# Kernel optimization log

Measured on AMD Instinct MI355X. Metric: run time of the kernel, lower is better.

Reference implementation:

```python
import jax, jax.numpy as jnp
import numpy as np

P = 1024
D_FF = 4096
TGT = 4096
SRC = 4096


def _ln(x, g, b, eps=1e-5):
    mu = jnp.mean(x, axis=-1, keepdims=True)
    var = jnp.mean((x - mu) ** 2, axis=-1, keepdims=True)
    return (x - mu) / jnp.sqrt(var + eps) * g + b


def setup_inputs() -> dict:
    key = jax.random.key(0)
    ks = jax.random.split(key, 32)
    s = 1.0 / np.sqrt(P)
    sf = 1.0 / np.sqrt(D_FF)
    d = {
        "Y": jax.random.normal(ks[0], (TGT, P), jnp.float32),
        "Xp": jax.random.normal(ks[1], (SRC, P), jnp.float32),
        # self-attn projections (Linear: y = x @ W + b, W stored [in, out])
        "wq1": jax.random.uniform(ks[2], (P, P), jnp.float32, -s, s),
        "bq1": jnp.zeros((P,), jnp.float32),
        "wk1": jax.random.uniform(ks[3], (P, P), jnp.float32, -s, s),
        "bk1": jnp.zeros((P,), jnp.float32),
        "wv1": jax.random.uniform(ks[4], (P, P), jnp.float32, -s, s),
        "bv1": jnp.zeros((P,), jnp.float32),
        "w0": jax.random.uniform(ks[5], (P, P), jnp.float32, -s, s),
        "b0": jnp.zeros((P,), jnp.float32),
        "g1": jnp.ones((P,), jnp.float32),
        "be1": jnp.zeros((P,), jnp.float32),
        # cross-attn projections
        "wq2": jax.random.uniform(ks[6], (P, P), jnp.float32, -s, s),
        "bq2": jnp.zeros((P,), jnp.float32),
        "wk2": jax.random.uniform(ks[7], (P, P), jnp.float32, -s, s),
        "bk2": jnp.zeros((P,), jnp.float32),
        "wv2": jax.random.uniform(ks[8], (P, P), jnp.float32, -s, s),
        "bv2": jnp.zeros((P,), jnp.float32),
        "w1": jax.random.uniform(ks[9], (P, P), jnp.float32, -s, s),
        "b1": jnp.zeros((P,), jnp.float32),
        "g2": jnp.ones((P,), jnp.float32),
        "be2": jnp.zeros((P,), jnp.float32),
        # FFN
        "w2": jax.random.uniform(ks[10], (P, D_FF), jnp.float32, -s, s),
        "b2": jnp.zeros((D_FF,), jnp.float32),
        "w3": jax.random.uniform(ks[11], (D_FF, P), jnp.float32, -sf, sf),
        "b3": jnp.zeros((P,), jnp.float32),
        "g3": jnp.ones((P,), jnp.float32),
        "be3": jnp.zeros((P,), jnp.float32),
    }
    return d


def reference(Y, Xp, wq1, bq1, wk1, bk1, wv1, bv1, w0, b0, g1, be1,
              wq2, bq2, wk2, bk2, wv2, bv2, w1, b1, g2, be2,
              w2, b2, w3, b3, g3, be3):
    m = Y.shape[0]
    scale = 1.0 / jnp.sqrt(jnp.asarray(P, Y.dtype))
    # --- masked self-attention on Y ---
    Q = Y @ wq1 + bq1            # [m, p]
    K = Y @ wk1 + bk1
    V = Y @ wv1 + bv1
    S = (Q @ K.T) * scale        # [m, m]
    causal = jnp.tril(jnp.ones((m, m), bool))
    S = jnp.where(causal, S, jnp.asarray(-1e9, S.dtype))
    A = jax.nn.softmax(S, axis=-1)
    T1 = (A @ V) @ w0 + b0
    U1 = _ln(Y + T1, g1, be1)
    # --- cross-attention with encoder output Xp ---
    Q = U1 @ wq2 + bq2           # [m, p]
    K = Xp @ wk2 + bk2           # [n, p]
    V = Xp @ wv2 + bv2
    S = (Q @ K.T) * scale        # [m, n]
    A = jax.nn.softmax(S, axis=-1)
    T2 = (A @ V) @ w1 + b1
    U2 = _ln(U1 + T2, g2, be2)
    # --- position-wise FFN ---
    Z = jax.nn.relu(U2 @ w2 + b2) @ w3 + b3
    U3 = _ln(U2 + Z, g3, be3)
    return U3
```

## Files before the change

kernel.cpp:

```cpp
#include <hip/hip_runtime.h>
#include <hip/hip_bf16.h>

typedef __bf16 bf16x8 __attribute__((ext_vector_type(8)));
typedef __bf16 bf16x4 __attribute__((ext_vector_type(4)));
typedef float f32x4 __attribute__((ext_vector_type(4)));

#define AS1P(p) ((__attribute__((address_space(1))) void*)(void*)(p))
#define AS3P(p) ((__attribute__((address_space(3))) void*)(p))

__global__ __launch_bounds__(256, 3) void gemm_bt(
    const __hip_bfloat16* __restrict__ A, int lda,
    const __hip_bfloat16* __restrict__ Bt, int ldb,
    int M, int N, int K, int ldc,
    const float* __restrict__ bias, int bias_mode,
    float scale,
    const float* __restrict__ residual,
    int relu, int causal_skip, int trapezoid, int ksplit,
    float* __restrict__ Cf, __hip_bfloat16* __restrict__ Cb,
    int nsplit1, const __hip_bfloat16* __restrict__ A2,
    const __hip_bfloat16* __restrict__ Bt2, int ldb2, int ldc2,
    const float* __restrict__ bias2, __hip_bfloat16* __restrict__ Cb2)
{
    int nb = blockIdx.x;
    int mb = blockIdx.y;
    {
        const int gx = gridDim.x, gy = gridDim.y;
        if ((gx & 3) == 0 && (gy & 1) == 0) {
            const int id = mb * gx + nb;
            const int X  = id & 7;
            const int L  = id >> 3;
            const int rn = gx >> 2, rm = gy >> 1;
            const int nb_l = L / rm, mb_l = L - nb_l * rm;
            nb = (X & 3) * rn + nb_l;
            mb = (X >> 2) * rm + mb_l;
        }
    }
    if (nsplit1 && nb >= nsplit1) {
        A = A2; Bt = Bt2; ldb = ldb2; ldc = ldc2; bias = bias2;
        Cb = Cb2; Cf = nullptr; residual = nullptr;
        nb -= nsplit1;
    }
    const int m_base = mb * 128;
    const int n_base = nb * 128;
    if (causal_skip && (n_base > m_base + 127)) return;
    int Kend = K;
    if (trapezoid) { int kl = m_base + 128; Kend = kl < K ? kl : K; }
    int kb = 0, ke = Kend;
    if (ksplit) {
        kb = blockIdx.z * ksplit;
        int k2 = kb + ksplit; ke = k2 < Kend ? k2 : Kend;
        if (kb >= ke) return;
        Cb += (size_t)blockIdx.z * M * ldc;
        Cf = nullptr;
    }
    const int nt = (ke - kb) >> 5;

    __shared__ __align__(16) __hip_bfloat16 Lds[3][8192];

    const int tid  = threadIdx.x;
    const int lane = tid & 63;
    const int wave = tid >> 6;
    const int wm = (wave >> 1) * 64;
    const int wn = (wave & 1) * 64;

    f32x4 acc[4][4];
#pragma unroll
    for (int i = 0; i < 4; ++i)
#pragma unroll
        for (int j = 0; j < 4; ++j) acc[i][j] = f32x4{0.f, 0.f, 0.f, 0.f};

    const bool isA = wave < 2;
    const __hip_bfloat16* G = isA ? (A + (size_t)m_base * lda) : (Bt + (size_t)n_base * ldb);
    const int ldg = isA ? lda : ldb;
    const int q0 = (wave & 1) * 4;
    const int rsub = lane >> 2;
    const int cx   = (lane & 3) ^ ((lane >> 3) & 3);
    const size_t grow = (size_t)(q0 * 16 + rsub) * ldg + (size_t)cx * 8 + kb;
    const int ldsoff = (isA ? 0 : 4096) + q0 * 512;

    const int lrow = lane & 15;
    const int cph  = ((lane >> 4) ^ ((lrow >> 1) & 3)) * 8;

#define ISSUE_TILE(KT, STG)                                                      \
    {                                                                            \
        const __hip_bfloat16* g = G + grow + (size_t)(KT) * 32;                  \
        __hip_bfloat16* dst = &Lds[STG][ldsoff];                                 \
        _Pragma("unroll")                                                        \
        for (int q = 0; q < 4; ++q) {                                            \
            __builtin_amdgcn_global_load_lds(AS1P(g), AS3P(dst), 16, 0, 0);      \
            g += (size_t)16 * ldg; dst += 512;                                   \
        }                                                                        \
    }

    ISSUE_TILE(0, 0)
    if (nt > 1) ISSUE_TILE(1, 1)

    int cur = 0;
    for (int kt = 0; kt < nt; ++kt) {
        __builtin_amdgcn_sched_barrier(0);
        if (kt + 1 < nt) __builtin_amdgcn_s_waitcnt(0x0F74);
        else             __builtin_amdgcn_s_waitcnt(0x0F70);
        __builtin_amdgcn_sched_barrier(0);
        __builtin_amdgcn_s_barrier();
        __builtin_amdgcn_sched_barrier(0);
        if (kt + 2 < nt) {
            int s2 = cur + 2; if (s2 >= 3) s2 -= 3;
            ISSUE_TILE(kt + 2, s2)
        }

        bf16x8 af[4], bfv[4];
#pragma unroll
        for (int i = 0; i < 4; ++i)
            af[i] = *(const bf16x8*)&Lds[cur][(wm + i * 16 + lrow) * 32 + cph];
#pragma unroll
        for (int j = 0; j < 4; ++j)
            bfv[j] = *(const bf16x8*)&Lds[cur][4096 + (wn + j * 16 + lrow) * 32 + cph];
#pragma unroll
        for (int i = 0; i < 4; ++i)
#pragma unroll
            for (int j = 0; j < 4; ++j)
                acc[i][j] = __builtin_amdgcn_mfma_f32_16x16x32_bf16(af[i], bfv[j], acc[i][j], 0, 0, 0);

        cur = (cur + 1 == 3) ? 0 : cur + 1;
    }
#undef ISSUE_TILE

    const int r0 = (lane >> 4) * 4;
    const int c0 = lane & 15;
#pragma unroll
    for (int i = 0; i < 4; ++i) {
#pragma unroll
        for (int j = 0; j < 4; ++j) {
            const int col = n_base + wn + j * 16 + c0;
#pragma unroll
            for (int r = 0; r < 4; ++r) {
                const int row = m_base + wm + i * 16 + r0 + r;
                float v = acc[i][j][r] * scale;
                if (bias_mode == 1) v += bias[col];
                else if (bias_mode == 2) v += bias[row];
                if (relu) v = fmaxf(v, 0.f);
                const size_t idx = (size_t)row * ldc + col;
                if (residual) v += residual[idx];
                if (Cf) Cf[idx] = v;
                else    Cb[idx] = __float2bfloat16(v);
            }
        }
    }
}

__global__ __launch_bounds__(256) void reduce_k_kernel(
    const __hip_bfloat16* __restrict__ Pb, int M, int N, int nsplit, int KC, int trapK,
    const float* __restrict__ bias, const float* __restrict__ residual,
    float* __restrict__ Cf, __hip_bfloat16* __restrict__ Cb)
{
    const int idx = blockIdx.x * 256 + threadIdx.x;
    const int nv = N >> 2;
    const int row = idx / nv;
    if (row >= M) return;
    const int c4 = (idx - row * nv) * 4;
    int nc = nsplit;
    if (trapK) {
        int kend = (row & ~127) + 128; if (kend > trapK) kend = trapK;
        nc = (kend + KC - 1) / KC;
    }
    float s0 = 0.f, s1 = 0.f, s2 = 0.f, s3 = 0.f;
    for (int c = 0; c < nc; ++c) {
        const bf16x4 p = *(const bf16x4*)(Pb + ((size_t)c * M + row) * N + c4);
        s0 += (float)p[0]; s1 += (float)p[1]; s2 += (float)p[2]; s3 += (float)p[3];
    }
    if (bias) {
        const f32x4 b = *(const f32x4*)(bias + c4);
        s0 += b[0]; s1 += b[1]; s2 += b[2]; s3 += b[3];
    }
    if (residual) {
        const f32x4 rv = *(const f32x4*)(residual + (size_t)row * N + c4);
        s0 += rv[0]; s1 += rv[1]; s2 += rv[2]; s3 += rv[3];
    }
    if (Cf) { f32x4 o = {s0, s1, s2, s3}; *(f32x4*)(Cf + (size_t)row * N + c4) = o; }
    else {
        bf16x4 o = { (__bf16)s0, (__bf16)s1, (__bf16)s2, (__bf16)s3 };
        *(bf16x4*)(Cb + (size_t)row * N + c4) = o;
    }
}

__global__ __launch_bounds__(256) void convert_bf16_kernel(
    const float* __restrict__ x, __hip_bfloat16* __restrict__ y, int n4)
{
    const int i = blockIdx.x * 256 + threadIdx.x;
    if (i >= n4) return;
    const float4 v = ((const float4*)x)[i];
    bf16x4 o = { (__bf16)v.x, (__bf16)v.y, (__bf16)v.z, (__bf16)v.w };
    *(bf16x4*)(y + (size_t)i * 4) = o;
}

__global__ __launch_bounds__(256) void transpose_convert_kernel(
    const float* __restrict__ W, __hip_bfloat16* __restrict__ Wt, int K, int N)
{
    __shared__ float t[32][33];
    const int k0 = blockIdx.y * 32;
    const int n0 = blockIdx.x * 32;
    const int tx = threadIdx.x;
    for (int i = threadIdx.y; i < 32; i += 8)
        t[i][tx] = W[(size_t)(k0 + i) * N + n0 + tx];
    __syncthreads();
    for (int i = threadIdx.y; i < 32; i += 8)
        Wt[(size_t)(n0 + i) * K + k0 + tx] = __float2bfloat16(t[tx][i]);
}

__global__ __launch_bounds__(256) void transpose_bf16_kernel(
    const __hip_bfloat16* __restrict__ src, int ls,
    __hip_bfloat16* __restrict__ dst, int ld)
{
    __shared__ __hip_bfloat16 t[32][33];
    const int r0 = blockIdx.y * 32;
    const int c0 = blockIdx.x * 32;
    const int tx = threadIdx.x;
    for (int i = threadIdx.y; i < 32; i += 8)
        t[i][tx] = src[(size_t)(r0 + i) * ls + c0 + tx];
    __syncthreads();
    for (int i = threadIdx.y; i < 32; i += 8)
        dst[(size_t)(c0 + i) * ld + r0 + tx] = t[tx][i];
}

__global__ __launch_bounds__(256) void softmax_kernel(
    const __hip_bfloat16* __restrict__ S, __hip_bfloat16* __restrict__ A, int N, int causal)
{
    __shared__ float sm[4];
    const int row = blockIdx.x;
    const int tid = threadIdx.x;
    const int limit = causal ? (row + 1) : N;
    const int zlimit = causal ? (((row & ~127) + 128) < N ? ((row & ~127) + 128) : N) : N;
    const __hip_bfloat16* Srow = S + (size_t)row * N;
    __hip_bfloat16* Arow = A + (size_t)row * N;
    const int nv = limit >> 2;

    float m = -3.0e38f;
    for (int v = tid; v < nv; v += 256) {
        const bf16x4 x = *(const bf16x4*)(Srow + (size_t)v * 4);
        m = fmaxf(m, fmaxf(fmaxf((float)x[0], (float)x[1]), fmaxf((float)x[2], (float)x[3])));
    }
    for (int j = (nv << 2) + tid; j < limit; j += 256) m = fmaxf(m, (float)Srow[j]);
#pragma unroll
    for (int o = 32; o; o >>= 1) m = fmaxf(m, __shfl_down(m, o));
    if ((tid & 63) == 0) sm[tid >> 6] = m;
    __syncthreads();
    m = fmaxf(fmaxf(sm[0], sm[1]), fmaxf(sm[2], sm[3]));
    __syncthreads();

    float s = 0.f;
    for (int v = tid; v < nv; v += 256) {
        const bf16x4 x = *(const bf16x4*)(Srow + (size_t)v * 4);
        s += __expf((float)x[0] - m) + __expf((float)x[1] - m)
           + __expf((float)x[2] - m) + __expf((float)x[3] - m);
    }
    for (int j = (nv << 2) + tid; j < limit; j += 256) s += __expf((float)Srow[j] - m);
#pragma unroll
    for (int o = 32; o; o >>= 1) s += __shfl_down(s, o);
    if ((tid & 63) == 0) sm[tid >> 6] = s;
    __syncthreads();
    s = sm[0] + sm[1] + sm[2] + sm[3];
    const float inv = 1.f / s;

    for (int v = tid; v < nv; v += 256) {
        const bf16x4 x = *(const bf16x4*)(Srow + (size_t)v * 4);
        bf16x4 o = { (__bf16)(__expf((float)x[0] - m) * inv), (__bf16)(__expf((float)x[1] - m) * inv),
                     (__bf16)(__expf((float)x[2] - m) * inv), (__bf16)(__expf((float)x[3] - m) * inv) };
        *(bf16x4*)(Arow + (size_t)v * 4) = o;
    }
    for (int j = (nv << 2) + tid; j < limit; j += 256)
        Arow[j] = __float2bfloat16(__expf((float)Srow[j] - m) * inv);
    const __hip_bfloat16 z = __float2bfloat16(0.f);
    for (int j = limit + tid; j < zlimit; j += 256) Arow[j] = z;
}

__global__ __launch_bounds__(256) void layernorm_kernel(
    const float* __restrict__ X, const float* __restrict__ g, const float* __restrict__ b,
    float* __restrict__ outF, __hip_bfloat16* __restrict__ outB)
{
    __shared__ float sm[8];
    const int row = blockIdx.x;
    const int tid = threadIdx.x;
    const float4 v = ((const float4*)(X + (size_t)row * 1024))[tid];
    float s  = v.x + v.y + v.z + v.w;
    float ss = v.x * v.x + v.y * v.y + v.z * v.z + v.w * v.w;
#pragma unroll
    for (int o = 32; o; o >>= 1) { s += __shfl_down(s, o); ss += __shfl_down(ss, o); }
    if ((tid & 63) == 0) { sm[tid >> 6] = s; sm[4 + (tid >> 6)] = ss; }
    __syncthreads();
    s  = sm[0] + sm[1] + sm[2] + sm[3];
    ss = sm[4] + sm[5] + sm[6] + sm[7];
    const float mu   = s * (1.f / 1024.f);
    const float var  = ss * (1.f / 1024.f) - mu * mu;
    const float rstd = rsqrtf(var + 1e-5f);
    const float4 gv = ((const float4*)g)[tid];
    const float4 bv = ((const float4*)b)[tid];
    float4 o;
    o.x = (v.x - mu) * rstd * gv.x + bv.x;
    o.y = (v.y - mu) * rstd * gv.y + bv.y;
    o.z = (v.z - mu) * rstd * gv.z + bv.z;
    o.w = (v.w - mu) * rstd * gv.w + bv.w;
    ((float4*)(outF + (size_t)row * 1024))[tid] = o;
    if (outB) {
        bf16x4 ob = { (__bf16)o.x, (__bf16)o.y, (__bf16)o.z, (__bf16)o.w };
        *(bf16x4*)(outB + (size_t)row * 1024 + (size_t)tid * 4) = ob;
    }
}

extern "C" void kernel_launch(void* const* d_in, const int* in_sizes, int n_in,
                              void* d_out, int out_size, void* d_ws, size_t ws_size,
                              hipStream_t stream)
{
    const int M = 4096, Pd = 1024, DFF = 4096, NS = 4096;
    const size_t MB = 1024 * 1024;

    const float* Y   = (const float*)d_in[0];
    const float* Xp  = (const float*)d_in[1];
    const float* wq1 = (const float*)d_in[2];  const float* bq1 = (const float*)d_in[3];
    const float* wk1 = (const float*)d_in[4];  const float* bk1 = (const float*)d_in[5];
    const float* wv1 = (const float*)d_in[6];  const float* bv1 = (const float*)d_in[7];
    const float* w0  = (const float*)d_in[8];  const float* b0  = (const float*)d_in[9];
    const float* g1  = (const float*)d_in[10]; const float* be1 = (const float*)d_in[11];
    const float* wq2 = (const float*)d_in[12]; const float* bq2 = (const float*)d_in[13];
    const float* wk2 = (const float*)d_in[14]; const float* bk2 = (const float*)d_in[15];
    const float* wv2 = (const float*)d_in[16]; const float* bv2 = (const float*)d_in[17];
    const float* w1  = (const float*)d_in[18]; const float* b1  = (const float*)d_in[19];
    const float* g2  = (const float*)d_in[20]; const float* be2 = (const float*)d_in[21];
    const float* w2  = (const float*)d_in[22]; const float* b2  = (const float*)d_in[23];
    const float* w3  = (const float*)d_in[24]; const float* b3  = (const float*)d_in[25];
    const float* g3  = (const float*)d_in[26]; const float* be3 = (const float*)d_in[27];

    char* ws = (char*)d_ws;
    __hip_bfloat16* Ybf   = (__hip_bfloat16*)(ws + 0 * MB);
    __hip_bfloat16* Ubf   = (__hip_bfloat16*)(ws + 0 * MB);
    __hip_bfloat16* Xpbf  = (__hip_bfloat16*)(ws + 8 * MB);
    __hip_bfloat16* AVbf  = (__hip_bfloat16*)(ws + 8 * MB);
    __hip_bfloat16* Qbf   = (__hip_bfloat16*)(ws + 8 * MB);
    __hip_bfloat16* wqkv1t= (__hip_bfloat16*)(ws + 16 * MB);
    __hip_bfloat16* w0t   = (__hip_bfloat16*)(ws + 22 * MB);
    __hip_bfloat16* wq2t  = (__hip_bfloat16*)(ws + 24 * MB);
    __hip_bfloat16* wkv2t = (__hip_bfloat16*)(ws + 26 * MB);
    __hip_bfloat16* w1t   = (__hip_bfloat16*)(ws + 30 * MB);
    __hip_bfloat16* w2t   = (__hip_bfloat16*)(ws + 32 * MB);
    __hip_bfloat16* w3t   = (__hip_bfloat16*)(ws + 40 * MB);
    float*          bqkv1 = (float*)(ws + 48 * MB);
    float*          bkv2  = (float*)(ws + 48 * MB + 512 * 1024);
    __hip_bfloat16* QKV1  = (__hip_bfloat16*)(ws + 49 * MB);
    __hip_bfloat16* KV2   = (__hip_bfloat16*)(ws + 73 * MB);
    __hip_bfloat16* Vt    = (__hip_bfloat16*)(ws + 89 * MB);
    __hip_bfloat16* Sb    = (__hip_bfloat16*)(ws + 97 * MB);
    __hip_bfloat16* Pb    = (__hip_bfloat16*)(ws + 97 * MB);
    __hip_bfloat16* Abf   = (__hip_bfloat16*)(ws + 161 * MB);
    float*          Xres  = (float*)(ws + 193 * MB);
    float*          Uf    = (float*)(ws + 209 * MB);
    float*          Out   = (float*)d_out;
    if (ws_size < 225 * MB) return;

    auto cvt = [&](const float* src, __hip_bfloat16* dst, int n) {
        convert_bf16_kernel<<<dim3(n / 1024), dim3(256), 0, stream>>>(src, dst, n / 4);
    };
    auto tconv = [&](const float* W, __hip_bfloat16* Wt, int K, int N) {
        transpose_convert_kernel<<<dim3(N / 32, K / 32), dim3(32, 8), 0, stream>>>(W, Wt, K, N);
    };
    auto tbf = [&](const __hip_bfloat16* src, int ls, __hip_bfloat16* dst, int ld, int R, int C) {
        transpose_bf16_kernel<<<dim3(C / 32, R / 32), dim3(32, 8), 0, stream>>>(src, ls, dst, ld);
    };
    auto gemm = [&](const __hip_bfloat16* A, int lda, const __hip_bfloat16* Bt, int ldb,
                    int Mm, int Nn, int Kk, int ldc,
                    const float* bias, int bmode, float scale, const float* res,
                    int relu, int causal, int trap, int ksplit,
                    float* Cf, __hip_bfloat16* Cb) {
        const int nz = ksplit ? (Kk + ksplit - 1) / ksplit : 1;
        gemm_bt<<<dim3(Nn / 128, Mm / 128, nz), dim3(256), 0, stream>>>(
            A, lda, Bt, ldb, Mm, Nn, Kk, ldc, bias, bmode, scale, res, relu, causal, trap, ksplit,
            Cf, Cb, 0, nullptr, nullptr, 0, 0, nullptr, nullptr);
    };
    auto reduce = [&](const __hip_bfloat16* P, int Mm, int Nn, int nsplit, int KC, int trapK,
                      const float* bias, const float* res, float* Cf, __hip_bfloat16* Cb) {
        reduce_k_kernel<<<dim3(Mm * Nn / 1024), dim3(256), 0, stream>>>(
            P, Mm, Nn, nsplit, KC, trapK, bias, res, Cf, Cb);
    };

    const float scl = 0.03125f;

    cvt(Y,  Ybf,  M * Pd);
    cvt(Xp, Xpbf, NS * Pd);
    tconv(wq1, wqkv1t,            Pd, Pd);
    tconv(wk1, wqkv1t + Pd * Pd,  Pd, Pd);
    tconv(wv1, wqkv1t + 2*Pd*Pd,  Pd, Pd);
    tconv(w0,  w0t,  Pd, Pd);
    tconv(wq2, wq2t, Pd, Pd);
    tconv(wk2, wkv2t,           Pd, Pd);
    tconv(wv2, wkv2t + Pd * Pd, Pd, Pd);
    tconv(w1,  w1t,  Pd, Pd);
    tconv(w2, w2t, Pd, DFF);
    tconv(w3, w3t, DFF, Pd);
    hipMemcpyAsync(bqkv1,            bq1, Pd * 4, hipMemcpyDeviceToDevice, stream);
    hipMemcpyAsync(bqkv1 + Pd,       bk1, Pd * 4, hipMemcpyDeviceToDevice, stream);
    hipMemcpyAsync(bqkv1 + 2 * Pd,   bv1, Pd * 4, hipMemcpyDeviceToDevice, stream);
    hipMemcpyAsync(bkv2,             bk2, Pd * 4, hipMemcpyDeviceToDevice, stream);
    hipMemcpyAsync(bkv2 + Pd,        bv2, Pd * 4, hipMemcpyDeviceToDevice, stream);

    gemm_bt<<<dim3(40, 32, 1), dim3(256), 0, stream>>>(
        Ybf, Pd, wqkv1t, Pd, M, 3072, Pd, 3072, bqkv1, 1, 1.f, nullptr, 0, 0, 0, 0,
        nullptr, QKV1,
        24, Xpbf, wkv2t, Pd, 2048, bkv2, KV2);

    tbf(QKV1 + 2048, 3072, Vt, M, M, Pd);
    gemm(QKV1, 3072, QKV1 + 1024, 3072, M, M, Pd, M,
         nullptr, 0, scl, nullptr, 0, 1, 0, 0, nullptr, Sb);
    softmax_kernel<<<dim3(M), dim3(256), 0, stream>>>(Sb, Abf, M, 1);
    gemm(Abf, M, Vt, M, M, Pd, M, Pd,
         nullptr, 0, 1.f, nullptr, 0, 0, 1, 1024, nullptr, Pb);
    reduce(Pb, M, Pd, 4, 1024, M, nullptr, nullptr, nullptr, AVbf);
    gemm(AVbf, Pd, w0t, Pd, M, Pd, Pd, Pd,
         nullptr, 0, 1.f, nullptr, 0, 0, 0, 512, nullptr, Pb);
    reduce(Pb, M, Pd, 2, 512, 0, b0, Y, Xres, nullptr);
    layernorm_kernel<<<dim3(M), dim3(256), 0, stream>>>(Xres, g1, be1, Uf, Ubf);

    gemm(Ubf, Pd, wq2t, Pd, M, Pd, Pd, Pd,
         nullptr, 0, 1.f, nullptr, 0, 0, 0, 512, nullptr, Pb);
    reduce(Pb, M, Pd, 2, 512, 0, bq2, nullptr, nullptr, Qbf);
    tbf(KV2 + 1024, 2048, Vt, NS, NS, Pd);
    gemm(Qbf, Pd, KV2, 2048, M, NS, Pd, NS,
         nullptr, 0, scl, nullptr, 0, 0, 0, 0, nullptr, Sb);
    softmax_kernel<<<dim3(M), dim3(256), 0, stream>>>(Sb, Abf, NS, 0);
    gemm(Abf, NS, Vt, NS, M, Pd, NS, Pd,
         nullptr, 0, 1.f, nullptr, 0, 0, 0, 1024, nullptr, Pb);
    reduce(Pb, M, Pd, 4, 1024, 0, nullptr, nullptr, nullptr, AVbf);
    gemm(AVbf, Pd, w1t, Pd, M, Pd, Pd, Pd,
         nullptr, 0, 1.f, nullptr, 0, 0, 0, 512, nullptr, Pb);
    reduce(Pb, M, Pd, 2, 512, 0, b1, Uf, Xres, nullptr);
    layernorm_kernel<<<dim3(M), dim3(256), 0, stream>>>(Xres, g2, be2, Uf, Ubf);

    gemm(Ubf, Pd, w2t, Pd, M, DFF, Pd, DFF, b2, 1, 1.f, nullptr, 1, 0, 0, 0, nullptr, Abf);
    gemm(Abf, DFF, w3t, DFF, M, Pd, DFF, Pd,
         nullptr, 0, 1.f, nullptr, 0, 0, 0, 1024, nullptr, Pb);
    reduce(Pb, M, Pd, 4, 1024, 0, b3, Uf, Xres, nullptr);
    layernorm_kernel<<<dim3(M), dim3(256), 0, stream>>>(Xres, g3, be3, Out, nullptr);
}
```

Measured before the change: 778.0 us.

## Add 256x128-tile GEMM kernel with grouped block swizzle for large GEMMs

```diff
diff --git a/kernel.cpp b/kernel.cpp
--- a/kernel.cpp
+++ b/kernel.cpp
@@ -148,6 +148,140 @@
     }
 }
 
+__global__ __launch_bounds__(256, 2) void gemm_bt2(
+    const __hip_bfloat16* __restrict__ A, int lda,
+    const __hip_bfloat16* __restrict__ Bt, int ldb,
+    int M, int N, int K, int ldc,
+    const float* __restrict__ bias, int bias_mode,
+    float scale,
+    int relu, int causal_skip, int trapezoid, int ksplit,
+    __hip_bfloat16* __restrict__ Cb)
+{
+    int nb = blockIdx.x;
+    int mb = blockIdx.y;
+    {
+        const int gx = gridDim.x, gy = gridDim.y;
+        if ((gx & 3) == 0 && (gy & 1) == 0) {
+            const int id = mb * gx + nb;
+            const int X  = id & 7;
+            const int L  = id >> 3;
+            const int rn = gx >> 2, rm = gy >> 1;
+            const int nb_l = L / rm, mb_l = L - nb_l * rm;
+            nb = (X & 3) * rn + nb_l;
+            mb = (X >> 2) * rm + mb_l;
+        }
+    }
+    const int m_base = mb * 256;
+    const int n_base = nb * 128;
+    if (causal_skip && (n_base > m_base + 255)) return;
+    int Kend = K;
+    if (trapezoid) { int kl = m_base + 256; Kend = kl < K ? kl : K; }
+    int kb = 0, ke = Kend;
+    if (ksplit) {
+        kb = blockIdx.z * ksplit;
+        int k2 = kb + ksplit; ke = k2 < Kend ? k2 : Kend;
+        if (kb >= ke) return;
+        Cb += (size_t)blockIdx.z * M * ldc;
+    }
+    const int nt = (ke - kb) >> 5;
+
+    __shared__ __align__(16) __hip_bfloat16 Lds[3][12288];
+
+    const int tid  = threadIdx.x;
+    const int lane = tid & 63;
+    const int wave = tid >> 6;
+    const int wm = wave * 64;
+    const int wtm = (wave >> 1) * 128;
+    const int wtn = (wave & 1) * 64;
+
+    f32x4 acc[8][4];
+#pragma unroll
+    for (int i = 0; i < 8; ++i)
+#pragma unroll
+        for (int j = 0; j < 4; ++j) acc[i][j] = f32x4{0.f, 0.f, 0.f, 0.f};
+
+    const int rsub = lane >> 2;
+    const int cx   = (lane & 3) ^ ((lane >> 3) & 3);
+    const __hip_bfloat16* GA = A  + (size_t)(m_base + wave * 64) * lda + (size_t)rsub * lda + (size_t)cx * 8 + kb;
+    const __hip_bfloat16* GB = Bt + (size_t)(n_base + wave * 32) * ldb + (size_t)rsub * ldb + (size_t)cx * 8 + kb;
+    const int ldsA = wave * 2048;
+    const int ldsB = 8192 + wave * 1024;
+
+    const int lrow = lane & 15;
+    const int cph  = ((lane >> 4) ^ ((lrow >> 1) & 3)) * 8;
+
+#define ISSUE_TILE2(KT, STG)                                                     \
+    {                                                                            \
+        const size_t ko = (size_t)(KT) * 32;                                     \
+        const __hip_bfloat16* ga = GA + ko;                                      \
+        __hip_bfloat16* da = &Lds[STG][ldsA];                                    \
+        _Pragma("unroll")                                                        \
+        for (int q = 0; q < 4; ++q) {                                            \
+            __builtin_amdgcn_global_load_lds(AS1P(ga), AS3P(da), 16, 0, 0);      \
+            ga += (size_t)16 * lda; da += 512;                                   \
+        }                                                                        \
+        const __hip_bfloat16* gb = GB + ko;                                      \
+        __hip_bfloat16* db = &Lds[STG][ldsB];                                    \
+        _Pragma("unroll")                                                        \
+        for (int q = 0; q < 2; ++q) {                                            \
+            __builtin_amdgcn_global_load_lds(AS1P(gb), AS3P(db), 16, 0, 0);      \
+            gb += (size_t)16 * ldb; db += 512;                                   \
+        }                                                                        \
+    }
+
+    ISSUE_TILE2(0, 0)
+    if (nt > 1) ISSUE_TILE2(1, 1)
+
+    int cur = 0;
+    for (int kt = 0; kt < nt; ++kt) {
+        __builtin_amdgcn_sched_barrier(0);
+        if (kt + 1 < nt) __builtin_amdgcn_s_waitcnt(0x0F76);
+        else             __builtin_amdgcn_s_waitcnt(0x0F70);
+        __builtin_amdgcn_sched_barrier(0);
+        __builtin_amdgcn_s_barrier();
+        __builtin_amdgcn_sched_barrier(0);
+        if (kt + 2 < nt) {
+            int s2 = cur + 2; if (s2 >= 3) s2 -= 3;
+            ISSUE_TILE2(kt + 2, s2)
+        }
+
+        bf16x8 af[8], bfv[4];
+#pragma unroll
+        for (int i = 0; i < 8; ++i)
+            af[i] = *(const bf16x8*)&Lds[cur][(wtm + i * 16 + lrow) * 32 + cph];
+#pragma unroll
+        for (int j = 0; j < 4; ++j)
+            bfv[j] = *(const bf16x8*)&Lds[cur][8192 + (wtn + j * 16 + lrow) * 32 + cph];
+#pragma unroll
+        for (int i = 0; i < 8; ++i)
+#pragma unroll
+            for (int j = 0; j < 4; ++j)
+                acc[i][j] = __builtin_amdgcn_mfma_f32_16x16x32_bf16(af[i], bfv[j], acc[i][j], 0, 0, 0);
+
+        cur = (cur + 1 == 3) ? 0 : cur + 1;
+    }
+#undef ISSUE_TILE2
+
+    const int r0 = (lane >> 4) * 4;
+    const int c0 = lane & 15;
+#pragma unroll
+    for (int i = 0; i < 8; ++i) {
+#pragma unroll
+        for (int j = 0; j < 4; ++j) {
+            const int col = n_base + wtn + j * 16 + c0;
+#pragma unroll
+            for (int r = 0; r < 4; ++r) {
+                const int row = m_base + wtm + i * 16 + r0 + r;
+                float v = acc[i][j][r] * scale;
+                if (bias_mode == 1) v += bias[col];
+                else if (bias_mode == 2) v += bias[row];
+                if (relu) v = fmaxf(v, 0.f);
+                Cb[(size_t)row * ldc + col] = __float2bfloat16(v);
+            }
+        }
+    }
+}
+
 __global__ __launch_bounds__(256) void reduce_k_kernel(
     const __hip_bfloat16* __restrict__ Pb, int M, int N, int nsplit, int KC, int trapK,
     const float* __restrict__ bias, const float* __restrict__ residual,
@@ -160,7 +294,7 @@
     const int c4 = (idx - row * nv) * 4;
     int nc = nsplit;
     if (trapK) {
-        int kend = (row & ~127) + 128; if (kend > trapK) kend = trapK;
+        int kend = (row & ~255) + 256; if (kend > trapK) kend = trapK;
         nc = (kend + KC - 1) / KC;
     }
     float s0 = 0.f, s1 = 0.f, s2 = 0.f, s3 = 0.f;
@@ -229,7 +363,7 @@
     const int row = blockIdx.x;
     const int tid = threadIdx.x;
     const int limit = causal ? (row + 1) : N;
-    const int zlimit = causal ? (((row & ~127) + 128) < N ? ((row & ~127) + 128) : N) : N;
+    const int zlimit = causal ? (((row & ~255) + 256) < N ? ((row & ~255) + 256) : N) : N;
     const __hip_bfloat16* Srow = S + (size_t)row * N;
     __hip_bfloat16* Arow = A + (size_t)row * N;
     const int nv = limit >> 2;
@@ -374,6 +508,14 @@
             A, lda, Bt, ldb, Mm, Nn, Kk, ldc, bias, bmode, scale, res, relu, causal, trap, ksplit,
             Cf, Cb, 0, nullptr, nullptr, 0, 0, nullptr, nullptr);
     };
+    auto gemm2 = [&](const __hip_bfloat16* A, int lda, const __hip_bfloat16* Bt, int ldb,
+                     int Mm, int Nn, int Kk, int ldc,
+                     const float* bias, int bmode, float scale,
+                     int relu, int causal, int trap, int ksplit, __hip_bfloat16* Cb) {
+        const int nz = ksplit ? (Kk + ksplit - 1) / ksplit : 1;
+        gemm_bt2<<<dim3(Nn / 128, Mm / 256, nz), dim3(256), 0, stream>>>(
+            A, lda, Bt, ldb, Mm, Nn, Kk, ldc, bias, bmode, scale, relu, causal, trap, ksplit, Cb);
+    };
     auto reduce = [&](const __hip_bfloat16* P, int Mm, int Nn, int nsplit, int KC, int trapK,
                       const float* bias, const float* res, float* Cf, __hip_bfloat16* Cb) {
         reduce_k_kernel<<<dim3(Mm * Nn / 1024), dim3(256), 0, stream>>>(
@@ -406,11 +548,11 @@
         24, Xpbf, wkv2t, Pd, 2048, bkv2, KV2);
 
     tbf(QKV1 + 2048, 3072, Vt, M, M, Pd);
-    gemm(QKV1, 3072, QKV1 + 1024, 3072, M, M, Pd, M,
-         nullptr, 0, scl, nullptr, 0, 1, 0, 0, nullptr, Sb);
+    gemm2(QKV1, 3072, QKV1 + 1024, 3072, M, M, Pd, M,
+          nullptr, 0, scl, 0, 1, 0, 0, Sb);
     softmax_kernel<<<dim3(M), dim3(256), 0, stream>>>(Sb, Abf, M, 1);
-    gemm(Abf, M, Vt, M, M, Pd, M, Pd,
-         nullptr, 0, 1.f, nullptr, 0, 0, 1, 1024, nullptr, Pb);
+    gemm2(Abf, M, Vt, M, M, Pd, M, Pd,
+          nullptr, 0, 1.f, 0, 0, 1, 1024, Pb);
     reduce(Pb, M, Pd, 4, 1024, M, nullptr, nullptr, nullptr, AVbf);
     gemm(AVbf, Pd, w0t, Pd, M, Pd, Pd, Pd,
          nullptr, 0, 1.f, nullptr, 0, 0, 0, 512, nullptr, Pb);
@@ -421,20 +563,20 @@
          nullptr, 0, 1.f, nullptr, 0, 0, 0, 512, nullptr, Pb);
     reduce(Pb, M, Pd, 2, 512, 0, bq2, nullptr, nullptr, Qbf);
     tbf(KV2 + 1024, 2048, Vt, NS, NS, Pd);
-    gemm(Qbf, Pd, KV2, 2048, M, NS, Pd, NS,
-         nullptr, 0, scl, nullptr, 0, 0, 0, 0, nullptr, Sb);
+    gemm2(Qbf, Pd, KV2, 2048, M, NS, Pd, NS,
+          nullptr, 0, scl, 0, 0, 0, 0, Sb);
     softmax_kernel<<<dim3(M), dim3(256), 0, stream>>>(Sb, Abf, NS, 0);
-    gemm(Abf, NS, Vt, NS, M, Pd, NS, Pd,
-         nullptr, 0, 1.f, nullptr, 0, 0, 0, 1024, nullptr, Pb);
+    gemm2(Abf, NS, Vt, NS, M, Pd, NS, Pd,
+          nullptr, 0, 1.f, 0, 0, 0, 1024, Pb);
     reduce(Pb, M, Pd, 4, 1024, 0, nullptr, nullptr, nullptr, AVbf);
     gemm(AVbf, Pd, w1t, Pd, M, Pd, Pd, Pd,
          nullptr, 0, 1.f, nullptr, 0, 0, 0, 512, nullptr, Pb);
     reduce(Pb, M, Pd, 2, 512, 0, b1, Uf, Xres, nullptr);
     layernorm_kernel<<<dim3(M), dim3(256), 0, stream>>>(Xres, g2, be2, Uf, Ubf);
 
-    gemm(Ubf, Pd, w2t, Pd, M, DFF, Pd, DFF, b2, 1, 1.f, nullptr, 1, 0, 0, 0, nullptr, Abf);
-    gemm(Abf, DFF, w3t, DFF, M, Pd, DFF, Pd,
-         nullptr, 0, 1.f, nullptr, 0, 0, 0, 1024, nullptr, Pb);
+    gemm2(Ubf, Pd, w2t, Pd, M, DFF, Pd, DFF, b2, 1, 1.f, 1, 0, 0, 0, Abf);
+    gemm2(Abf, DFF, w3t, DFF, M, Pd, DFF, Pd,
+          nullptr, 0, 1.f, 0, 0, 0, 1024, Pb);
     reduce(Pb, M, Pd, 4, 1024, 0, b3, Uf, Xres, nullptr);
     layernorm_kernel<<<dim3(M), dim3(256), 0, stream>>>(Xres, g3, be3, Out, nullptr);
 }
```

New measurement: 751.2 us. -3.4%, faster.
